# Kernel tuning notes

Measured on AMD Instinct MI355X. Metric: run time of the kernel, lower is better.

The kernel has to match this reference:

```python
import jax, jax.numpy as jnp
import numpy as np

N, E, IN, H, K = 50000, 800000, 64, 128, 16
EPS = 1e-15


def setup_inputs() -> dict:
    key = jax.random.key(0)
    ks = jax.random.split(key, 8)
    x = jax.random.normal(ks[0], (N, IN), jnp.float32)
    edge_index = jax.random.randint(ks[1], (2, E), 0, N)
    edge_weight = jax.random.uniform(ks[2], (E,), jnp.float32)
    # GCNConv(normalize=False) params: lin weight (no lin bias) + additive bias
    W1 = jax.random.normal(ks[3], (IN, H), jnp.float32) / np.sqrt(IN)
    b1 = jnp.zeros((H,), jnp.float32)
    W2 = jax.random.normal(ks[4], (H, H), jnp.float32) / np.sqrt(H)
    b2 = jnp.zeros((H,), jnp.float32)
    # MLP head: single Linear(H, K) since mlp_units=[]
    Wm = jax.random.normal(ks[5], (H, K), jnp.float32) / np.sqrt(H)
    bm = jnp.zeros((K,), jnp.float32)
    return {"x": x, "edge_index": edge_index, "edge_weight": edge_weight,
            "W1": W1, "b1": b1, "W2": W2, "b2": b2, "Wm": Wm, "bm": bm}


def _gcn(h_in, W, b, src, dst, w):
    # GCNConv with normalize=False, cached=False: no self-loops, no degree norm.
    # out_i = sum_{(j->i) in E} w_ji * (x_j @ W) + b
    h = h_in @ W                         # [N, out] dense transform first
    msg = h[src] * w[:, None]            # [E, out] gather + edge scale
    agg = jax.ops.segment_sum(msg, dst, num_segments=N)  # scatter-add
    return agg + b


def reference(x, edge_index, edge_weight, W1, b1, W2, b2, Wm, bm):
    src, dst = edge_index[0], edge_index[1]
    h = jax.nn.relu(_gcn(x, W1, b1, src, dst, edge_weight))
    h = jax.nn.relu(_gcn(h, W2, b2, src, dst, edge_weight))
    s = h @ Wm + bm                      # cluster logits [N, K]
    sm = jax.nn.softmax(s, axis=-1)      # soft assignments S
    # just_balance_pool balance loss: -trace(sqrt(S^T S + EPS)) elementwise-sqrt,
    # i.e. -sum_k sqrt(sum_i S_ik^2 + EPS), normalized by sqrt(N*K).
    diag = jnp.sum(sm * sm, axis=0)      # [K] = diag(S^T S)
    loss = -jnp.sum(jnp.sqrt(diag + EPS))
    loss = loss / jnp.sqrt(jnp.asarray(N * K, sm.dtype))
    return sm, loss
```

## Files before the change

### kernel.cpp

```cpp
#include <hip/hip_runtime.h>
#include <hip/hip_fp16.h>
#include <math.h>

static constexpr int N_NODES = 50000;
static constexpr int E_EDGES = 800000;
static constexpr int IN_F = 64;
static constexpr int H_F = 128;
static constexpr int K_C = 16;
static constexpr int SCAN_B = 1024;
static constexpr int NB = (N_NODES + SCAN_B - 1) / SCAN_B;
static constexpr int BUCK_SHIFT = 7;
static constexpr int NBUCK = (N_NODES + 127) >> BUCK_SHIFT;
static constexpr int CHUNK_E = 4096;
static constexpr int NCHUNK = (E_EDGES + CHUNK_E - 1) / CHUNK_E;
static constexpr int BUCK_CAP = 4096;

typedef _Float16 h4 __attribute__((ext_vector_type(4)));
typedef _Float16 h8 __attribute__((ext_vector_type(8)));
typedef float f4 __attribute__((ext_vector_type(4)));

__device__ __forceinline__ void unpack(unsigned int e, int& s, float& w) {
  s = (int)(e & 0xffffu);
  w = __half2float(__ushort_as_half((unsigned short)(e >> 16)));
}

__global__ __launch_bounds__(256) void prep_kernel(
    const float* __restrict__ x, __half* __restrict__ xh,
    const float* __restrict__ W1, __half* __restrict__ WT1,
    const float* __restrict__ W2, __half* __restrict__ WT2,
    int* __restrict__ deg, float* __restrict__ diag) {
  const int i = blockIdx.x * 256 + threadIdx.x;
  const int n4 = N_NODES * IN_F / 4;
  if (i < n4) {
    float4 v = ((const float4*)x)[i];
    __half2* o = (__half2*)xh + (size_t)i * 2;
    o[0] = __floats2half2_rn(v.x, v.y);
    o[1] = __floats2half2_rn(v.z, v.w);
  }
  const int j = i - n4;
  if (j >= 0 && j < IN_F * 128) {
    const int k = j >> 7, col = j & 127;
    unsigned boff = (unsigned)((col * IN_F + k) * 2) ^ (unsigned)((col & 7) << 4);
    *(__half*)((char*)WT1 + boff) = __float2half_rn(W1[j]);
  }
  const int k2 = j - IN_F * 128;
  if (k2 >= 0 && k2 < H_F * 128) {
    const int k = k2 >> 7, col = k2 & 127;
    unsigned boff = (unsigned)((col * H_F + k) * 2) ^ (unsigned)((col & 7) << 4);
    *(__half*)((char*)WT2 + boff) = __float2half_rn(W2[k2]);
  }
  if (i < N_NODES) deg[i] = 0;
  if (i < K_C) diag[i] = 0.f;
}

__global__ __launch_bounds__(256) void hist_kernel(
    const int* __restrict__ dst, int* __restrict__ deg) {
  int e = blockIdx.x * 256 + threadIdx.x;
  if (e < E_EDGES) atomicAdd(&deg[dst[e]], 1);
}

__global__ __launch_bounds__(1024) void scan_local(
    const int* __restrict__ deg, int* __restrict__ off, int* __restrict__ blockSum) {
  __shared__ int part[SCAN_B];
  const int tid = threadIdx.x;
  const int i = blockIdx.x * SCAN_B + tid;
  const int v = (i < N_NODES) ? deg[i] : 0;
  part[tid] = v;
  __syncthreads();
  for (int d = 1; d < SCAN_B; d <<= 1) {
    int add = (tid >= d) ? part[tid - d] : 0;
    __syncthreads();
    part[tid] += add;
    __syncthreads();
  }
  if (i < N_NODES) off[i] = part[tid] - v;
  if (tid == SCAN_B - 1) blockSum[blockIdx.x] = part[tid];
}

__global__ __launch_bounds__(1024) void add_base(
    int* __restrict__ off, const int* __restrict__ blockSum, int* __restrict__ bcursor) {
  __shared__ int base_s;
  if (threadIdx.x < 64) {
    const int t = threadIdx.x;
    int v = (t < NB) ? blockSum[t] : 0;
    int inc = v;
#pragma unroll
    for (int d = 1; d < 64; d <<= 1) {
      int u = __shfl_up(inc, d);
      if (t >= d) inc += u;
    }
    if (t == (int)blockIdx.x) base_s = inc - v;
  }
  __syncthreads();
  const int i = blockIdx.x * SCAN_B + threadIdx.x;
  if (i < N_NODES) {
    int o = off[i] + base_s;
    off[i] = o;
    if ((i & 127) == 0) bcursor[i >> BUCK_SHIFT] = o;
  }
  if (i == 0) off[N_NODES] = E_EDGES;
}

__global__ __launch_bounds__(256) void bin_pass(
    const int* __restrict__ src, const int* __restrict__ dst,
    const float* __restrict__ w, int* __restrict__ bcursor,
    int2* __restrict__ inter) {
  __shared__ int lhist[NBUCK];
  __shared__ int lstart[NBUCK];
  __shared__ int bbase[NBUCK];
  __shared__ int2 stage[CHUNK_E];
  const int e0 = blockIdx.x * CHUNK_E;
  const int cnt = min(CHUNK_E, E_EDGES - e0);

  for (int i = threadIdx.x; i < NBUCK; i += 256) lhist[i] = 0;
  __syncthreads();
  for (int i = threadIdx.x; i < cnt; i += 256)
    atomicAdd(&lhist[dst[e0 + i] >> BUCK_SHIFT], 1);
  __syncthreads();

  if (threadIdx.x < 64) {
    const int lane = threadIdx.x;
    int carry = 0;
    for (int base = 0; base < NBUCK; base += 64) {
      const int idx = base + lane;
      const int v = (idx < NBUCK) ? lhist[idx] : 0;
      int inc = v;
#pragma unroll
      for (int d = 1; d < 64; d <<= 1) {
        int u = __shfl_up(inc, d);
        if (lane >= d) inc += u;
      }
      if (idx < NBUCK) lstart[idx] = carry + inc - v;
      carry += __shfl(inc, 63);
    }
  }
  __syncthreads();

  for (int b = threadIdx.x; b < NBUCK; b += 256) {
    const int c = lhist[b];
    bbase[b] = (c > 0) ? atomicAdd(&bcursor[b], c) : 0;
    lhist[b] = lstart[b];
  }
  __syncthreads();

  for (int i = threadIdx.x; i < cnt; i += 256) {
    const int d = dst[e0 + i];
    const int b = d >> BUCK_SHIFT;
    const int pos = atomicAdd(&lhist[b], 1);
    const unsigned short wb = __half_as_ushort(__float2half_rn(w[e0 + i]));
    stage[pos] = make_int2(src[e0 + i] | ((d & 127) << 16),
                           (int)wb | (b << 16));
  }
  __syncthreads();

  for (int i = threadIdx.x; i < cnt; i += 256) {
    const int2 en = stage[i];
    const int b = (en.y >> 16) & 0x1ff;
    inter[bbase[b] + (i - lstart[b])] = en;
  }
}

__global__ __launch_bounds__(256) void sort_pass(
    const int2* __restrict__ inter, const int* __restrict__ off,
    unsigned int* __restrict__ csr) {
  __shared__ int lcur[128];
  __shared__ unsigned int outbuf[BUCK_CAP];
  const int b = blockIdx.x;
  const int n0 = b << BUCK_SHIFT;
  const int r0 = off[n0];
  const int nend = min(n0 + 128, N_NODES);
  const int r1 = off[nend];
  const int cnt = r1 - r0;
  if (threadIdx.x < 128) {
    const int nn = n0 + threadIdx.x;
    lcur[threadIdx.x] = ((nn < N_NODES) ? off[nn] : r1) - r0;
  }
  __syncthreads();
  for (int i = threadIdx.x; i < cnt; i += 256) {
    const int2 en = inter[r0 + i];
    const int dlo = (en.x >> 16) & 127;
    const int pos = atomicAdd(&lcur[dlo], 1);
    outbuf[pos] = (unsigned int)(en.x & 0xffff) |
                  ((unsigned int)(en.y & 0xffff) << 16);
  }
  __syncthreads();
  for (int i = threadIdx.x; i < cnt; i += 256) csr[r0 + i] = outbuf[i];
}

__global__ __launch_bounds__(256) void gather_x(
    const __half* __restrict__ t, const int* __restrict__ off,
    const unsigned int* __restrict__ csr, __half* __restrict__ outb) {
  const int node = blockIdx.x * 4 + (threadIdx.x >> 6);
  const int l = threadIdx.x & 63;
  const int g = l >> 4;
  const int f0 = (l & 15) * 4;
  const int p0 = off[node], p1 = off[node + 1];
  f4 a0 = {0.f, 0.f, 0.f, 0.f}, a1 = {0.f, 0.f, 0.f, 0.f};
  int p = p0;
  for (; p + 8 <= p1; p += 8) {
    unsigned e0 = csr[p + g], e1 = csr[p + 4 + g];
    int s0, s1; float w0, w1;
    unpack(e0, s0, w0); unpack(e1, s1, w1);
    const h4 v0 = *(const h4*)(t + (size_t)s0 * IN_F + f0);
    const h4 v1 = *(const h4*)(t + (size_t)s1 * IN_F + f0);
    a0.x = fmaf((float)v0.x, w0, a0.x); a0.y = fmaf((float)v0.y, w0, a0.y);
    a0.z = fmaf((float)v0.z, w0, a0.z); a0.w = fmaf((float)v0.w, w0, a0.w);
    a1.x = fmaf((float)v1.x, w1, a1.x); a1.y = fmaf((float)v1.y, w1, a1.y);
    a1.z = fmaf((float)v1.z, w1, a1.z); a1.w = fmaf((float)v1.w, w1, a1.w);
  }
  for (; p < p1; p += 4) {
    const int idx = p + g;
    unsigned e = csr[min(idx, p1 - 1)];
    int s; float w;
    unpack(e, s, w);
    if (idx >= p1) w = 0.f;
    const h4 v = *(const h4*)(t + (size_t)s * IN_F + f0);
    a0.x = fmaf((float)v.x, w, a0.x); a0.y = fmaf((float)v.y, w, a0.y);
    a0.z = fmaf((float)v.z, w, a0.z); a0.w = fmaf((float)v.w, w, a0.w);
  }
  a0.x += a1.x; a0.y += a1.y; a0.z += a1.z; a0.w += a1.w;
  a0.x += __shfl_xor(a0.x, 16); a0.y += __shfl_xor(a0.y, 16);
  a0.z += __shfl_xor(a0.z, 16); a0.w += __shfl_xor(a0.w, 16);
  a0.x += __shfl_xor(a0.x, 32); a0.y += __shfl_xor(a0.y, 32);
  a0.z += __shfl_xor(a0.z, 32); a0.w += __shfl_xor(a0.w, 32);
  if (l < 16) {
    h4 o;
    o.x = (_Float16)a0.x; o.y = (_Float16)a0.y;
    o.z = (_Float16)a0.z; o.w = (_Float16)a0.w;
    *(h4*)(outb + (size_t)node * IN_F + f0) = o;
  }
}

template<int K, bool BIAS_RELU>
__global__ __launch_bounds__(256) void gemm_mfma(
    const __half* __restrict__ A, const __half* __restrict__ WT,
    const float* __restrict__ bias, __half* __restrict__ out, int n) {
  __shared__ _Float16 Wl[128 * K];
  for (int t = threadIdx.x; t < 128 * K / 8; t += 256)
    ((uint4*)Wl)[t] = ((const uint4*)WT)[t];
  __syncthreads();

  const int wv = threadIdx.x >> 6;
  const int l = threadIdx.x & 63;
  const int row = l & 15, kg = l >> 4;
  const int r0 = blockIdx.x * 64 + wv * 16;
  const int ar = min(r0 + row, n - 1);

  h8 af[K / 32];
#pragma unroll
  for (int ks = 0; ks < K / 32; ++ks)
    af[ks] = *(const h8*)(A + (size_t)ar * K + ks * 32 + kg * 8);

  const unsigned swz = (unsigned)((row & 7) << 4);
#pragma unroll
  for (int c = 0; c < 8; ++c) {
    const int col = c * 16 + row;
    f4 acc = {0.f, 0.f, 0.f, 0.f};
#pragma unroll
    for (int ks = 0; ks < K / 32; ++ks) {
      const unsigned boff = ((unsigned)((col * K + ks * 32 + kg * 8) * 2)) ^ swz;
      const h8 bf = *(const h8*)((const char*)Wl + boff);
      acc = __builtin_amdgcn_mfma_f32_16x16x32_f16(af[ks], bf, acc, 0, 0, 0);
    }
    const float bb = BIAS_RELU ? bias[col] : 0.f;
#pragma unroll
    for (int q = 0; q < 4; ++q) {
      const int rr = r0 + kg * 4 + q;
      if (rr < n) {
        float v = acc[q];
        if (BIAS_RELU) v = fmaxf(v + bb, 0.f);
        out[(size_t)rr * H_F + col] = __float2half_rn(v);
      }
    }
  }
}

__global__ __launch_bounds__(256) void gather_h(
    const __half* __restrict__ t, const int* __restrict__ off,
    const unsigned int* __restrict__ csr, __half* __restrict__ outb) {
  const int node = blockIdx.x * 4 + (threadIdx.x >> 6);
  const int lane = threadIdx.x & 63;
  const __half2* __restrict__ tb = (const __half2*)t;
  const int p0 = off[node], p1 = off[node + 1];
  float2 a0 = make_float2(0.f, 0.f), a1 = make_float2(0.f, 0.f);
  float2 a2 = make_float2(0.f, 0.f), a3 = make_float2(0.f, 0.f);
  int p = p0;
  for (; p + 8 <= p1; p += 8) {
    int s0, s1, s2, s3, s4, s5, s6, s7;
    float w0, w1, w2, w3, w4, w5, w6, w7;
    unpack(csr[p], s0, w0);     unpack(csr[p + 1], s1, w1);
    unpack(csr[p + 2], s2, w2); unpack(csr[p + 3], s3, w3);
    unpack(csr[p + 4], s4, w4); unpack(csr[p + 5], s5, w5);
    unpack(csr[p + 6], s6, w6); unpack(csr[p + 7], s7, w7);
    const __half2 h0 = tb[(size_t)s0 * 64 + lane];
    const __half2 h1 = tb[(size_t)s1 * 64 + lane];
    const __half2 h2 = tb[(size_t)s2 * 64 + lane];
    const __half2 h3 = tb[(size_t)s3 * 64 + lane];
    const __half2 h4 = tb[(size_t)s4 * 64 + lane];
    const __half2 h5 = tb[(size_t)s5 * 64 + lane];
    const __half2 h6 = tb[(size_t)s6 * 64 + lane];
    const __half2 h7 = tb[(size_t)s7 * 64 + lane];
    float2 f;
    f = __half22float2(h0); a0.x = fmaf(f.x, w0, a0.x); a0.y = fmaf(f.y, w0, a0.y);
    f = __half22float2(h1); a1.x = fmaf(f.x, w1, a1.x); a1.y = fmaf(f.y, w1, a1.y);
    f = __half22float2(h2); a2.x = fmaf(f.x, w2, a2.x); a2.y = fmaf(f.y, w2, a2.y);
    f = __half22float2(h3); a3.x = fmaf(f.x, w3, a3.x); a3.y = fmaf(f.y, w3, a3.y);
    f = __half22float2(h4); a0.x = fmaf(f.x, w4, a0.x); a0.y = fmaf(f.y, w4, a0.y);
    f = __half22float2(h5); a1.x = fmaf(f.x, w5, a1.x); a1.y = fmaf(f.y, w5, a1.y);
    f = __half22float2(h6); a2.x = fmaf(f.x, w6, a2.x); a2.y = fmaf(f.y, w6, a2.y);
    f = __half22float2(h7); a3.x = fmaf(f.x, w7, a3.x); a3.y = fmaf(f.y, w7, a3.y);
  }
  for (; p < p1; ++p) {
    int s; float w;
    unpack(csr[p], s, w);
    const float2 f = __half22float2(tb[(size_t)s * 64 + lane]);
    a0.x = fmaf(f.x, w, a0.x); a0.y = fmaf(f.y, w, a0.y);
  }
  const float2 s = make_float2((a0.x + a1.x) + (a2.x + a3.x),
                               (a0.y + a1.y) + (a2.y + a3.y));
  ((__half2*)outb)[(size_t)node * 64 + lane] = __float22half2_rn(s);
}

__global__ __launch_bounds__(256) void head_kernel(
    const __half* __restrict__ h2raw, const float* __restrict__ b2,
    const float* __restrict__ Wm, const float* __restrict__ bm,
    float* __restrict__ sm_out, float* __restrict__ diag, int n) {
  __shared__ float Wl[H_F * K_C];
  __shared__ float b2l[H_F];
  __shared__ float part[K_C];
  for (int t = threadIdx.x; t < H_F * K_C; t += 256) Wl[t] = Wm[t];
  if (threadIdx.x < H_F) b2l[threadIdx.x] = b2[threadIdx.x];
  if (threadIdx.x < K_C) part[threadIdx.x] = 0.f;
  __syncthreads();

  const int node = blockIdx.x * 256 + threadIdx.x;
  const int lane = threadIdx.x & 63;
  float acc[K_C];
#pragma unroll
  for (int c = 0; c < K_C; ++c) acc[c] = bm[c];

  if (node < n) {
    const __half2* __restrict__ hrow = (const __half2*)(h2raw + (size_t)node * H_F);
#pragma unroll 4
    for (int k2 = 0; k2 < H_F / 2; ++k2) {
      const float2 hv = __half22float2(hrow[k2]);
      const float h0 = fmaxf(hv.x + b2l[2 * k2], 0.f);
      const float h1 = fmaxf(hv.y + b2l[2 * k2 + 1], 0.f);
      const float4* __restrict__ w0 = (const float4*)(Wl + (2 * k2) * K_C);
      const float4* __restrict__ w1 = (const float4*)(Wl + (2 * k2 + 1) * K_C);
#pragma unroll
      for (int q = 0; q < 4; ++q) {
        const float4 a = w0[q], b = w1[q];
        acc[4 * q + 0] = fmaf(h0, a.x, acc[4 * q + 0]);
        acc[4 * q + 1] = fmaf(h0, a.y, acc[4 * q + 1]);
        acc[4 * q + 2] = fmaf(h0, a.z, acc[4 * q + 2]);
        acc[4 * q + 3] = fmaf(h0, a.w, acc[4 * q + 3]);
        acc[4 * q + 0] = fmaf(h1, b.x, acc[4 * q + 0]);
        acc[4 * q + 1] = fmaf(h1, b.y, acc[4 * q + 1]);
        acc[4 * q + 2] = fmaf(h1, b.z, acc[4 * q + 2]);
        acc[4 * q + 3] = fmaf(h1, b.w, acc[4 * q + 3]);
      }
    }
  }

  float mx = acc[0];
#pragma unroll
  for (int c = 1; c < K_C; ++c) mx = fmaxf(mx, acc[c]);
  float sum = 0.f;
#pragma unroll
  for (int c = 0; c < K_C; ++c) { acc[c] = __expf(acc[c] - mx); sum += acc[c]; }
  const float inv = 1.f / sum;
  float sq[K_C];
  if (node < n) {
#pragma unroll
    for (int c = 0; c < K_C; ++c) { acc[c] *= inv; sq[c] = acc[c] * acc[c]; }
    float4* o = (float4*)(sm_out + (size_t)node * K_C);
    o[0] = make_float4(acc[0], acc[1], acc[2], acc[3]);
    o[1] = make_float4(acc[4], acc[5], acc[6], acc[7]);
    o[2] = make_float4(acc[8], acc[9], acc[10], acc[11]);
    o[3] = make_float4(acc[12], acc[13], acc[14], acc[15]);
  } else {
#pragma unroll
    for (int c = 0; c < K_C; ++c) sq[c] = 0.f;
  }

#pragma unroll
  for (int c = 0; c < K_C; ++c) {
    float v = sq[c];
#pragma unroll
    for (int off = 32; off; off >>= 1) v += __shfl_xor(v, off);
    if (lane == 0) atomicAdd(&part[c], v);
  }
  __syncthreads();
  if (threadIdx.x < K_C) atomicAdd(&diag[threadIdx.x], part[threadIdx.x]);
}

__global__ void loss_kernel(const float* __restrict__ diag, float* __restrict__ out) {
  int c = threadIdx.x;
  float v = (c < K_C) ? sqrtf(diag[c] + 1e-15f) : 0.f;
#pragma unroll
  for (int off = 8; off; off >>= 1) v += __shfl_xor(v, off, 16);
  if (c == 0) out[0] = -v / sqrtf((float)N_NODES * (float)K_C);
}

extern "C" void kernel_launch(void* const* d_in, const int* in_sizes, int n_in,
                              void* d_out, int out_size, void* d_ws, size_t ws_size,
                              hipStream_t stream) {
  const float* x  = (const float*)d_in[0];
  const int*   ei = (const int*)d_in[1];
  const float* ew = (const float*)d_in[2];
  const float* W1 = (const float*)d_in[3];
  const float* b1 = (const float*)d_in[4];
  const float* W2 = (const float*)d_in[5];
  const float* b2 = (const float*)d_in[6];
  const float* Wm = (const float*)d_in[7];
  const float* bm = (const float*)d_in[8];
  float* out = (float*)d_out;

  const int* srcv = ei;
  const int* dstv = ei + E_EDGES;

  char* ws = (char*)d_ws;
  float*        diag    = (float*)ws;
  int*          bsum    = (int*)(ws + 256);
  int*          bcursor = (int*)(ws + 512);
  __half*       WT1     = (__half*)(ws + 4096);
  __half*       WT2     = (__half*)(ws + 4096 + 16384);
  int*          off     = (int*)(ws + 57344);
  int*          deg     = off + (N_NODES + 64);
  unsigned int* csr     = (unsigned int*)(deg + N_NODES);
  int2*         inter   = (int2*)(csr + E_EDGES);
  char*         bufA    = (char*)(inter + E_EDGES);
  char*         bufB    = bufA + (size_t)N_NODES * H_F * 2;

  __half* xh    = (__half*)bufB;
  __half* aggxh = (__half*)bufA;
  __half* h1h   = (__half*)bufB;
  __half* t2h   = (__half*)bufA;
  __half* h2h   = (__half*)bufB;

  prep_kernel<<<3221, 256, 0, stream>>>(x, xh, W1, WT1, W2, WT2, deg, diag);

  hist_kernel<<<(E_EDGES + 255) / 256, 256, 0, stream>>>(dstv, deg);
  scan_local<<<NB, SCAN_B, 0, stream>>>(deg, off, bsum);
  add_base<<<NB, SCAN_B, 0, stream>>>(off, bsum, bcursor);
  bin_pass<<<NCHUNK, 256, 0, stream>>>(srcv, dstv, ew, bcursor, inter);
  sort_pass<<<NBUCK, 256, 0, stream>>>(inter, off, csr);

  gather_x<<<N_NODES / 4, 256, 0, stream>>>(xh, off, csr, aggxh);
  gemm_mfma<IN_F, true><<<(N_NODES + 63) / 64, 256, 0, stream>>>(aggxh, WT1, b1, h1h, N_NODES);

  gemm_mfma<H_F, false><<<(N_NODES + 63) / 64, 256, 0, stream>>>(h1h, WT2, nullptr, t2h, N_NODES);
  gather_h<<<N_NODES / 4, 256, 0, stream>>>(t2h, off, csr, h2h);

  head_kernel<<<(N_NODES + 255) / 256, 256, 0, stream>>>(h2h, b2, Wm, bm, out, diag, N_NODES);
  loss_kernel<<<1, 64, 0, stream>>>(diag, out + (size_t)N_NODES * K_C);
}
```

Before: 176.7 us.

## Replace per-node degree histogram and scan with bucket histogram; unroll gathers

The CSR build no longer does a global per-node atomic histogram followed by a two-kernel 50K-element scan. It now counts edges per 128-node bucket using shared-memory histograms, scans the 391 bucket counts in one wavefront, and computes per-node offsets inside the bucket sort kernel from a local histogram. The gather kernels also get a 16-edge unrolled loop so more independent loads are in flight. This removes two kernel launches and 800K global atomics, at the cost of an extra pass over the bucketed edges in the sort kernel and higher register pressure in the gathers.

```diff
diff --git a/kernel.cpp b/kernel.cpp
--- a/kernel.cpp
+++ b/kernel.cpp
@@ -7,8 +7,6 @@
 static constexpr int IN_F = 64;
 static constexpr int H_F = 128;
 static constexpr int K_C = 16;
-static constexpr int SCAN_B = 1024;
-static constexpr int NB = (N_NODES + SCAN_B - 1) / SCAN_B;
 static constexpr int BUCK_SHIFT = 7;
 static constexpr int NBUCK = (N_NODES + 127) >> BUCK_SHIFT;
 static constexpr int CHUNK_E = 4096;
@@ -28,7 +26,7 @@
     const float* __restrict__ x, __half* __restrict__ xh,
     const float* __restrict__ W1, __half* __restrict__ WT1,
     const float* __restrict__ W2, __half* __restrict__ WT2,
-    int* __restrict__ deg, float* __restrict__ diag) {
+    int* __restrict__ bcount, float* __restrict__ diag) {
   const int i = blockIdx.x * 256 + threadIdx.x;
   const int n4 = N_NODES * IN_F / 4;
   if (i < n4) {
@@ -49,56 +47,45 @@
     unsigned boff = (unsigned)((col * H_F + k) * 2) ^ (unsigned)((col & 7) << 4);
     *(__half*)((char*)WT2 + boff) = __float2half_rn(W2[k2]);
   }
-  if (i < N_NODES) deg[i] = 0;
+  if (i < NBUCK) bcount[i] = 0;
   if (i < K_C) diag[i] = 0.f;
 }
 
-__global__ __launch_bounds__(256) void hist_kernel(
-    const int* __restrict__ dst, int* __restrict__ deg) {
-  int e = blockIdx.x * 256 + threadIdx.x;
-  if (e < E_EDGES) atomicAdd(&deg[dst[e]], 1);
-}
-
-__global__ __launch_bounds__(1024) void scan_local(
-    const int* __restrict__ deg, int* __restrict__ off, int* __restrict__ blockSum) {
-  __shared__ int part[SCAN_B];
-  const int tid = threadIdx.x;
-  const int i = blockIdx.x * SCAN_B + tid;
-  const int v = (i < N_NODES) ? deg[i] : 0;
-  part[tid] = v;
-  __syncthreads();
-  for (int d = 1; d < SCAN_B; d <<= 1) {
-    int add = (tid >= d) ? part[tid - d] : 0;
-    __syncthreads();
-    part[tid] += add;
-    __syncthreads();
-  }
-  if (i < N_NODES) off[i] = part[tid] - v;
-  if (tid == SCAN_B - 1) blockSum[blockIdx.x] = part[tid];
-}
-
-__global__ __launch_bounds__(1024) void add_base(
-    int* __restrict__ off, const int* __restrict__ blockSum, int* __restrict__ bcursor) {
-  __shared__ int base_s;
-  if (threadIdx.x < 64) {
-    const int t = threadIdx.x;
-    int v = (t < NB) ? blockSum[t] : 0;
+__global__ __launch_bounds__(256) void bhist_kernel(
+    const int* __restrict__ dst, int* __restrict__ bcount) {
+  __shared__ int lh[NBUCK];
+  for (int i = threadIdx.x; i < NBUCK; i += 256) lh[i] = 0;
+  __syncthreads();
+  const int e0 = blockIdx.x * CHUNK_E;
+  const int cnt = min(CHUNK_E, E_EDGES - e0);
+  for (int i = threadIdx.x; i < cnt; i += 256)
+    atomicAdd(&lh[dst[e0 + i] >> BUCK_SHIFT], 1);
+  __syncthreads();
+  for (int i = threadIdx.x; i < NBUCK; i += 256)
+    if (lh[i]) atomicAdd(&bcount[i], lh[i]);
+}
+
+__global__ __launch_bounds__(64) void bscan_kernel(
+    const int* __restrict__ bcount, int* __restrict__ bbase, int* __restrict__ bcursor) {
+  const int t = threadIdx.x;
+  int carry = 0;
+  for (int base = 0; base < NBUCK; base += 64) {
+    const int idx = base + t;
+    const int v = (idx < NBUCK) ? bcount[idx] : 0;
     int inc = v;
 #pragma unroll
     for (int d = 1; d < 64; d <<= 1) {
       int u = __shfl_up(inc, d);
       if (t >= d) inc += u;
     }
-    if (t == (int)blockIdx.x) base_s = inc - v;
-  }
-  __syncthreads();
-  const int i = blockIdx.x * SCAN_B + threadIdx.x;
-  if (i < N_NODES) {
-    int o = off[i] + base_s;
-    off[i] = o;
-    if ((i & 127) == 0) bcursor[i >> BUCK_SHIFT] = o;
-  }
-  if (i == 0) off[N_NODES] = E_EDGES;
+    if (idx < NBUCK) {
+      const int ex = carry + inc - v;
+      bbase[idx] = ex;
+      bcursor[idx] = ex;
+    }
+    carry += __shfl(inc, 63);
+  }
+  if (t == 0) bbase[NBUCK] = E_EDGES;
 }
 
 __global__ __launch_bounds__(256) void bin_pass(
@@ -107,7 +94,7 @@
     int2* __restrict__ inter) {
   __shared__ int lhist[NBUCK];
   __shared__ int lstart[NBUCK];
-  __shared__ int bbase[NBUCK];
+  __shared__ int bbase_s[NBUCK];
   __shared__ int2 stage[CHUNK_E];
   const int e0 = blockIdx.x * CHUNK_E;
   const int cnt = min(CHUNK_E, E_EDGES - e0);
@@ -138,7 +125,7 @@
 
   for (int b = threadIdx.x; b < NBUCK; b += 256) {
     const int c = lhist[b];
-    bbase[b] = (c > 0) ? atomicAdd(&bcursor[b], c) : 0;
+    bbase_s[b] = (c > 0) ? atomicAdd(&bcursor[b], c) : 0;
     lhist[b] = lstart[b];
   }
   __syncthreads();
@@ -156,30 +143,58 @@
   for (int i = threadIdx.x; i < cnt; i += 256) {
     const int2 en = stage[i];
     const int b = (en.y >> 16) & 0x1ff;
-    inter[bbase[b] + (i - lstart[b])] = en;
-  }
-}
-
-__global__ __launch_bounds__(256) void sort_pass(
-    const int2* __restrict__ inter, const int* __restrict__ off,
-    unsigned int* __restrict__ csr) {
-  __shared__ int lcur[128];
+    inter[bbase_s[b] + (i - lstart[b])] = en;
+  }
+}
+
+__global__ __launch_bounds__(256) void sortoff_pass(
+    const int2* __restrict__ inter, const int* __restrict__ bbase,
+    unsigned int* __restrict__ csr, int* __restrict__ off) {
+  __shared__ int lhist[128];
+  __shared__ int lstart[128];
   __shared__ unsigned int outbuf[BUCK_CAP];
   const int b = blockIdx.x;
   const int n0 = b << BUCK_SHIFT;
-  const int r0 = off[n0];
-  const int nend = min(n0 + 128, N_NODES);
-  const int r1 = off[nend];
+  const int r0 = bbase[b];
+  const int r1 = bbase[b + 1];
   const int cnt = r1 - r0;
+
+  if (threadIdx.x < 128) lhist[threadIdx.x] = 0;
+  __syncthreads();
+  for (int i = threadIdx.x; i < cnt; i += 256)
+    atomicAdd(&lhist[(inter[r0 + i].x >> 16) & 127], 1);
+  __syncthreads();
+
+  if (threadIdx.x < 64) {
+    const int lane = threadIdx.x;
+    int carry = 0;
+#pragma unroll
+    for (int base = 0; base < 128; base += 64) {
+      const int v = lhist[base + lane];
+      int inc = v;
+#pragma unroll
+      for (int d = 1; d < 64; d <<= 1) {
+        int u = __shfl_up(inc, d);
+        if (lane >= d) inc += u;
+      }
+      lstart[base + lane] = carry + inc - v;
+      carry += __shfl(inc, 63);
+    }
+  }
+  __syncthreads();
+
   if (threadIdx.x < 128) {
     const int nn = n0 + threadIdx.x;
-    lcur[threadIdx.x] = ((nn < N_NODES) ? off[nn] : r1) - r0;
-  }
-  __syncthreads();
+    if (nn < N_NODES) off[nn] = r0 + lstart[threadIdx.x];
+    lhist[threadIdx.x] = lstart[threadIdx.x];
+  }
+  if (b == NBUCK - 1 && threadIdx.x == 0) off[N_NODES] = E_EDGES;
+  __syncthreads();
+
   for (int i = threadIdx.x; i < cnt; i += 256) {
     const int2 en = inter[r0 + i];
     const int dlo = (en.x >> 16) & 127;
-    const int pos = atomicAdd(&lcur[dlo], 1);
+    const int pos = atomicAdd(&lhist[dlo], 1);
     outbuf[pos] = (unsigned int)(en.x & 0xffff) |
                   ((unsigned int)(en.y & 0xffff) << 16);
   }
@@ -197,10 +212,22 @@
   const int p0 = off[node], p1 = off[node + 1];
   f4 a0 = {0.f, 0.f, 0.f, 0.f}, a1 = {0.f, 0.f, 0.f, 0.f};
   int p = p0;
+  for (; p + 16 <= p1; p += 16) {
+    int s[4]; float w[4]; h4 v[4];
+#pragma unroll
+    for (int u = 0; u < 4; ++u) unpack(csr[p + 4 * u + g], s[u], w[u]);
+#pragma unroll
+    for (int u = 0; u < 4; ++u) v[u] = *(const h4*)(t + (size_t)s[u] * IN_F + f0);
+#pragma unroll
+    for (int u = 0; u < 4; ++u) {
+      f4& a = (u & 1) ? a1 : a0;
+      a.x = fmaf((float)v[u].x, w[u], a.x); a.y = fmaf((float)v[u].y, w[u], a.y);
+      a.z = fmaf((float)v[u].z, w[u], a.z); a.w = fmaf((float)v[u].w, w[u], a.w);
+    }
+  }
   for (; p + 8 <= p1; p += 8) {
-    unsigned e0 = csr[p + g], e1 = csr[p + 4 + g];
     int s0, s1; float w0, w1;
-    unpack(e0, s0, w0); unpack(e1, s1, w1);
+    unpack(csr[p + g], s0, w0); unpack(csr[p + 4 + g], s1, w1);
     const h4 v0 = *(const h4*)(t + (size_t)s0 * IN_F + f0);
     const h4 v1 = *(const h4*)(t + (size_t)s1 * IN_F + f0);
     a0.x = fmaf((float)v0.x, w0, a0.x); a0.y = fmaf((float)v0.y, w0, a0.y);
@@ -282,43 +309,45 @@
   const int lane = threadIdx.x & 63;
   const __half2* __restrict__ tb = (const __half2*)t;
   const int p0 = off[node], p1 = off[node + 1];
-  float2 a0 = make_float2(0.f, 0.f), a1 = make_float2(0.f, 0.f);
-  float2 a2 = make_float2(0.f, 0.f), a3 = make_float2(0.f, 0.f);
+  float2 a[4];
+#pragma unroll
+  for (int i = 0; i < 4; ++i) a[i] = make_float2(0.f, 0.f);
   int p = p0;
+  for (; p + 16 <= p1; p += 16) {
+    int s[16]; float w[16]; __half2 hv[16];
+#pragma unroll
+    for (int i = 0; i < 16; ++i) unpack(csr[p + i], s[i], w[i]);
+#pragma unroll
+    for (int i = 0; i < 16; ++i) hv[i] = tb[(size_t)s[i] * 64 + lane];
+#pragma unroll
+    for (int i = 0; i < 16; ++i) {
+      const float2 f = __half22float2(hv[i]);
+      a[i & 3].x = fmaf(f.x, w[i], a[i & 3].x);
+      a[i & 3].y = fmaf(f.y, w[i], a[i & 3].y);
+    }
+  }
   for (; p + 8 <= p1; p += 8) {
-    int s0, s1, s2, s3, s4, s5, s6, s7;
-    float w0, w1, w2, w3, w4, w5, w6, w7;
-    unpack(csr[p], s0, w0);     unpack(csr[p + 1], s1, w1);
-    unpack(csr[p + 2], s2, w2); unpack(csr[p + 3], s3, w3);
-    unpack(csr[p + 4], s4, w4); unpack(csr[p + 5], s5, w5);
-    unpack(csr[p + 6], s6, w6); unpack(csr[p + 7], s7, w7);
-    const __half2 h0 = tb[(size_t)s0 * 64 + lane];
-    const __half2 h1 = tb[(size_t)s1 * 64 + lane];
-    const __half2 h2 = tb[(size_t)s2 * 64 + lane];
-    const __half2 h3 = tb[(size_t)s3 * 64 + lane];
-    const __half2 h4 = tb[(size_t)s4 * 64 + lane];
-    const __half2 h5 = tb[(size_t)s5 * 64 + lane];
-    const __half2 h6 = tb[(size_t)s6 * 64 + lane];
-    const __half2 h7 = tb[(size_t)s7 * 64 + lane];
-    float2 f;
-    f = __half22float2(h0); a0.x = fmaf(f.x, w0, a0.x); a0.y = fmaf(f.y, w0, a0.y);
-    f = __half22float2(h1); a1.x = fmaf(f.x, w1, a1.x); a1.y = fmaf(f.y, w1, a1.y);
-    f = __half22float2(h2); a2.x = fmaf(f.x, w2, a2.x); a2.y = fmaf(f.y, w2, a2.y);
-    f = __half22float2(h3); a3.x = fmaf(f.x, w3, a3.x); a3.y = fmaf(f.y, w3, a3.y);
-    f = __half22float2(h4); a0.x = fmaf(f.x, w4, a0.x); a0.y = fmaf(f.y, w4, a0.y);
-    f = __half22float2(h5); a1.x = fmaf(f.x, w5, a1.x); a1.y = fmaf(f.y, w5, a1.y);
-    f = __half22float2(h6); a2.x = fmaf(f.x, w6, a2.x); a2.y = fmaf(f.y, w6, a2.y);
-    f = __half22float2(h7); a3.x = fmaf(f.x, w7, a3.x); a3.y = fmaf(f.y, w7, a3.y);
+    int s[8]; float w[8]; __half2 hv[8];
+#pragma unroll
+    for (int i = 0; i < 8; ++i) unpack(csr[p + i], s[i], w[i]);
+#pragma unroll
+    for (int i = 0; i < 8; ++i) hv[i] = tb[(size_t)s[i] * 64 + lane];
+#pragma unroll
+    for (int i = 0; i < 8; ++i) {
+      const float2 f = __half22float2(hv[i]);
+      a[i & 3].x = fmaf(f.x, w[i], a[i & 3].x);
+      a[i & 3].y = fmaf(f.y, w[i], a[i & 3].y);
+    }
   }
   for (; p < p1; ++p) {
     int s; float w;
     unpack(csr[p], s, w);
     const float2 f = __half22float2(tb[(size_t)s * 64 + lane]);
-    a0.x = fmaf(f.x, w, a0.x); a0.y = fmaf(f.y, w, a0.y);
-  }
-  const float2 s = make_float2((a0.x + a1.x) + (a2.x + a3.x),
-                               (a0.y + a1.y) + (a2.y + a3.y));
-  ((__half2*)outb)[(size_t)node * 64 + lane] = __float22half2_rn(s);
+    a[0].x = fmaf(f.x, w, a[0].x); a[0].y = fmaf(f.y, w, a[0].y);
+  }
+  const float2 s2 = make_float2((a[0].x + a[1].x) + (a[2].x + a[3].x),
+                                (a[0].y + a[1].y) + (a[2].y + a[3].y));
+  ((__half2*)outb)[(size_t)node * 64 + lane] = __float22half2_rn(s2);
 }
 
 __global__ __launch_bounds__(256) void head_kernel(
@@ -350,15 +379,15 @@
       const float4* __restrict__ w1 = (const float4*)(Wl + (2 * k2 + 1) * K_C);
 #pragma unroll
       for (int q = 0; q < 4; ++q) {
-        const float4 a = w0[q], b = w1[q];
-        acc[4 * q + 0] = fmaf(h0, a.x, acc[4 * q + 0]);
-        acc[4 * q + 1] = fmaf(h0, a.y, acc[4 * q + 1]);
-        acc[4 * q + 2] = fmaf(h0, a.z, acc[4 * q + 2]);
-        acc[4 * q + 3] = fmaf(h0, a.w, acc[4 * q + 3]);
-        acc[4 * q + 0] = fmaf(h1, b.x, acc[4 * q + 0]);
-        acc[4 * q + 1] = fmaf(h1, b.y, acc[4 * q + 1]);
-        acc[4 * q + 2] = fmaf(h1, b.z, acc[4 * q + 2]);
-        acc[4 * q + 3] = fmaf(h1, b.w, acc[4 * q + 3]);
+        const float4 aa = w0[q], bb = w1[q];
+        acc[4 * q + 0] = fmaf(h0, aa.x, acc[4 * q + 0]);
+        acc[4 * q + 1] = fmaf(h0, aa.y, acc[4 * q + 1]);
+        acc[4 * q + 2] = fmaf(h0, aa.z, acc[4 * q + 2]);
+        acc[4 * q + 3] = fmaf(h0, aa.w, acc[4 * q + 3]);
+        acc[4 * q + 0] = fmaf(h1, bb.x, acc[4 * q + 0]);
+        acc[4 * q + 1] = fmaf(h1, bb.y, acc[4 * q + 1]);
+        acc[4 * q + 2] = fmaf(h1, bb.z, acc[4 * q + 2]);
+        acc[4 * q + 3] = fmaf(h1, bb.w, acc[4 * q + 3]);
       }
     }
   }
@@ -388,7 +417,7 @@
   for (int c = 0; c < K_C; ++c) {
     float v = sq[c];
 #pragma unroll
-    for (int off = 32; off; off >>= 1) v += __shfl_xor(v, off);
+    for (int off2 = 32; off2; off2 >>= 1) v += __shfl_xor(v, off2);
     if (lane == 0) atomicAdd(&part[c], v);
   }
   __syncthreads();
@@ -399,7 +428,7 @@
   int c = threadIdx.x;
   float v = (c < K_C) ? sqrtf(diag[c] + 1e-15f) : 0.f;
 #pragma unroll
-  for (int off = 8; off; off >>= 1) v += __shfl_xor(v, off, 16);
+  for (int off2 = 8; off2; off2 >>= 1) v += __shfl_xor(v, off2, 16);
   if (c == 0) out[0] = -v / sqrtf((float)N_NODES * (float)K_C);
 }
 
@@ -422,13 +451,13 @@
 
   char* ws = (char*)d_ws;
   float*        diag    = (float*)ws;
-  int*          bsum    = (int*)(ws + 256);
-  int*          bcursor = (int*)(ws + 512);
-  __half*       WT1     = (__half*)(ws + 4096);
-  __half*       WT2     = (__half*)(ws + 4096 + 16384);
-  int*          off     = (int*)(ws + 57344);
-  int*          deg     = off + (N_NODES + 64);
-  unsigned int* csr     = (unsigned int*)(deg + N_NODES);
+  int*          bcount  = (int*)(ws + 256);
+  int*          bbase   = (int*)(ws + 2048);
+  int*          bcursor = (int*)(ws + 4096);
+  __half*       WT1     = (__half*)(ws + 8192);
+  __half*       WT2     = (__half*)(ws + 8192 + 16384);
+  int*          off     = (int*)(ws + 65536);
+  unsigned int* csr     = (unsigned int*)(off + N_NODES + 64);
   int2*         inter   = (int2*)(csr + E_EDGES);
   char*         bufA    = (char*)(inter + E_EDGES);
   char*         bufB    = bufA + (size_t)N_NODES * H_F * 2;
@@ -439,13 +468,12 @@
   __half* t2h   = (__half*)bufA;
   __half* h2h   = (__half*)bufB;
 
-  prep_kernel<<<3221, 256, 0, stream>>>(x, xh, W1, WT1, W2, WT2, deg, diag);
-
-  hist_kernel<<<(E_EDGES + 255) / 256, 256, 0, stream>>>(dstv, deg);
-  scan_local<<<NB, SCAN_B, 0, stream>>>(deg, off, bsum);
-  add_base<<<NB, SCAN_B, 0, stream>>>(off, bsum, bcursor);
+  prep_kernel<<<3221, 256, 0, stream>>>(x, xh, W1, WT1, W2, WT2, bcount, diag);
+
+  bhist_kernel<<<NCHUNK, 256, 0, stream>>>(dstv, bcount);
+  bscan_kernel<<<1, 64, 0, stream>>>(bcount, bbase, bcursor);
   bin_pass<<<NCHUNK, 256, 0, stream>>>(srcv, dstv, ew, bcursor, inter);
-  sort_pass<<<NBUCK, 256, 0, stream>>>(inter, off, csr);
+  sortoff_pass<<<NBUCK, 256, 0, stream>>>(inter, bbase, csr, off);
 
   gather_x<<<N_NODES / 4, 256, 0, stream>>>(xh, off, csr, aggxh);
   gemm_mfma<IN_F, true><<<(N_NODES + 63) / 64, 256, 0, stream>>>(aggxh, WT1, b1, h1h, N_NODES);
```

Measured after the change: 153.5 us. 13.1% less time.
